# Performance work log

Measured on AMD Instinct MI355X. Metric: run time of the kernel, lower is better.

Reference implementation:

```python
import jax, jax.numpy as jnp
import numpy as np

HIDDEN = 512
X_SIZE = 128
S_SIZE = 64


def _lstm_cell(h, c, inp, Wi, Wh, bi, bh):
    # PyTorch gate order: i, f, g, o
    gates = inp @ Wi.T + bi + h @ Wh.T + bh  # [B, 4H]
    i, f, g, o = jnp.split(gates, 4, axis=-1)
    c = jax.nn.sigmoid(f) * c + jax.nn.sigmoid(i) * jnp.tanh(g)
    h = jax.nn.sigmoid(o) * jnp.tanh(c)
    return h, c


def setup_inputs() -> dict:
    key = jax.random.key(0)
    ks = jax.random.split(key, 16)
    B, T, H = 256, 512, HIDDEN
    in0 = X_SIZE + S_SIZE
    sc0 = 1.0 / np.sqrt(H)
    d = {
        "x": jax.random.normal(ks[0], (B, T, X_SIZE), jnp.float32),
        "s0": jax.random.normal(ks[1], (B, S_SIZE), jnp.float32),
        "W_ih0": jax.random.uniform(ks[2], (4 * H, in0), jnp.float32, -sc0, sc0),
        "W_hh0": jax.random.uniform(ks[3], (4 * H, H), jnp.float32, -sc0, sc0),
        "b_ih0": jax.random.uniform(ks[4], (4 * H,), jnp.float32, -sc0, sc0),
        "b_hh0": jax.random.uniform(ks[5], (4 * H,), jnp.float32, -sc0, sc0),
        "W_ih1": jax.random.uniform(ks[6], (4 * H, H), jnp.float32, -sc0, sc0),
        "W_hh1": jax.random.uniform(ks[7], (4 * H, H), jnp.float32, -sc0, sc0),
        "b_ih1": jax.random.uniform(ks[8], (4 * H,), jnp.float32, -sc0, sc0),
        "b_hh1": jax.random.uniform(ks[9], (4 * H,), jnp.float32, -sc0, sc0),
        "W_fc": jax.random.uniform(ks[10], (S_SIZE, H), jnp.float32, -sc0, sc0),
        "b_fc": jax.random.uniform(ks[11], (S_SIZE,), jnp.float32, -sc0, sc0),
        "seq_length": 512,
    }
    return d


def reference(x, s0, W_ih0, W_hh0, b_ih0, b_hh0, W_ih1, W_hh1, b_ih1, b_hh1,
              W_fc, b_fc, seq_length):
    B = x.shape[0]
    H = W_hh0.shape[1]
    zeros = jnp.zeros((B, H), x.dtype)

    def step(carry, x_t):
        h0, c0, h1, c1, s = carry
        inp = jnp.concatenate([x_t, s], axis=-1)  # [B, x_size + s_size]
        h0, c0 = _lstm_cell(h0, c0, inp, W_ih0, W_hh0, b_ih0, b_hh0)
        h1, c1 = _lstm_cell(h1, c1, h0, W_ih1, W_hh1, b_ih1, b_hh1)
        out = h1 @ W_fc.T + b_fc  # [B, s_size]
        s = s + out               # residual state update
        return (h0, c0, h1, c1, s), out

    xs = jnp.swapaxes(x[:, :seq_length], 0, 1)  # time-major [T, B, x_size]
    _, outs = jax.lax.scan(step, (zeros, zeros, zeros, zeros, s0), xs)
    return jnp.swapaxes(outs, 0, 1)  # [B, T, s_size]
```

## Files before the change

kernel.cpp:

```cpp
#include <hip/hip_runtime.h>
#include <cstdint>
#include <cstddef>

typedef __bf16 bf16;
typedef _Float16 f16;
typedef __bf16 bf16x8 __attribute__((ext_vector_type(8)));
typedef _Float16 f16x8 __attribute__((ext_vector_type(8)));
typedef float  f32x4  __attribute__((ext_vector_type(4)));
typedef unsigned int uint2v __attribute__((ext_vector_type(2)));
typedef unsigned int uint4v __attribute__((ext_vector_type(4)));
typedef unsigned long long u64;

constexpr int B_=256, T_=512, H_=512, X_=128, S_=64, IN0=192;
constexpr int NG=2;
constexpr int MG=128;
constexpr int WPG=128;
constexpr int KB_X=4, KB_H=16, KB_S=2;
constexpr float LOSCL = 4096.0f, INV_LOSCL = 1.0f/4096.0f;

constexpr size_t OFF_FLG=0;
constexpr size_t OFF_BC =16384;
constexpr size_t OFF_SC =32768;
constexpr size_t OFF_HP =OFF_SC+2ull*NG*64*128*4;
constexpr size_t PLANE  =2ull*B_*H_*2;
constexpr size_t WS_NEED=OFF_HP+2*PLANE;

constexpr int NWX=KB_X*512;
constexpr int NWH=KB_H*512;
constexpr int NWS=KB_S*512;
constexpr int SMEM_BYTES = (2*NWX + 8*NWH + 2*NWS)*2
                         + 2*512*2 + 128*17*4 + 512*2 + 32*4;
static_assert(SMEM_BYTES == 155264, "lds size");
static_assert(SMEM_BYTES <= 160*1024, "lds limit");

__device__ __forceinline__ uint4v ald16(const void* p) {
  uint4v r;
  asm volatile("global_load_dwordx4 %0, %1, off sc1"
               : "=&v"(r) : "v"(p) : "memory");
  return r;
}
__device__ __forceinline__ f16x8 MKF(uint4v q) {
  union { uint4v q; f16x8 v; } u; u.q = q;
  return u.v;
}
__device__ __forceinline__ void astore8(void* p, uint2v v) {
  union { uint2v v; u64 q; } u; u.v = v;
  __hip_atomic_store((u64*)p, u.q, __ATOMIC_RELAXED, __HIP_MEMORY_SCOPE_AGENT);
}
__device__ __forceinline__ void astoref(float* p, float v) {
  __hip_atomic_store((unsigned*)p, __float_as_uint(v), __ATOMIC_RELAXED, __HIP_MEMORY_SCOPE_AGENT);
}
__device__ __forceinline__ float aloadf(const float* p) {
  return __uint_as_float(__hip_atomic_load((unsigned*)p, __ATOMIC_RELAXED, __HIP_MEMORY_SCOPE_AGENT));
}

__device__ __forceinline__ f32x4 mfmaB(bf16x8 a, bf16x8 b, f32x4 c) {
  return __builtin_amdgcn_mfma_f32_16x16x32_bf16(a, b, c, 0, 0, 0);
}
__device__ __forceinline__ f32x4 mfmaF(f16x8 a, f16x8 b, f32x4 c) {
  return __builtin_amdgcn_mfma_f32_16x16x32_f16(a, b, c, 0, 0, 0);
}
__device__ __forceinline__ f32x4 mfma3(bf16x8 ah, bf16x8 al, bf16x8 wh, bf16x8 wl, f32x4 c) {
  c = mfmaB(ah, wh, c);
  c = mfmaB(al, wh, c);
  c = mfmaB(ah, wl, c);
  return c;
}
__device__ __forceinline__ void split8p(const float* v, bf16x8& ah, bf16x8& al) {
  #pragma unroll
  for (int i=0;i<8;++i){ float f=v[i]; bf16 h=(bf16)f; ah[i]=h; al[i]=(bf16)(f-(float)h); }
}
__device__ __forceinline__ void split8v(f32x4 v0, f32x4 v1, bf16x8& ah, bf16x8& al) {
  #pragma unroll
  for (int i=0;i<4;++i){ float f=v0[i]; bf16 h=(bf16)f; ah[i]=h; al[i]=(bf16)(f-(float)h); }
  #pragma unroll
  for (int i=0;i<4;++i){ float f=v1[i]; bf16 h=(bf16)f; ah[4+i]=h; al[4+i]=(bf16)(f-(float)h); }
}
__device__ __forceinline__ float sigm(float v) { return 1.0f / (1.0f + __expf(-v)); }
__device__ __forceinline__ float tanhr(float v) {
  v = fminf(15.0f, fmaxf(-15.0f, v));
  float e = __expf(2.0f * v);
  return (e - 1.0f) / (e + 1.0f);
}

__device__ __forceinline__ void group_barrier(int* flg, int* bc, int ns, int& phase) {
  ++phase;
  const int p = phase;
  asm volatile("s_waitcnt vmcnt(0)" ::: "memory");
  __syncthreads();
  if (threadIdx.x == 0)
    __hip_atomic_store(flg + ns*16, p, __ATOMIC_RELAXED, __HIP_MEMORY_SCOPE_AGENT);
  if (ns == 0) {
    if (threadIdx.x < WPG) {
      while (__hip_atomic_load(flg + (int)threadIdx.x*16, __ATOMIC_RELAXED,
                               __HIP_MEMORY_SCOPE_AGENT) < p)
        __builtin_amdgcn_s_sleep(1);
    }
    __syncthreads();
    if (threadIdx.x == 0)
      __hip_atomic_store(bc, p, __ATOMIC_RELAXED, __HIP_MEMORY_SCOPE_AGENT);
  }
  if (threadIdx.x == 0) {
    while (__hip_atomic_load(bc, __ATOMIC_RELAXED, __HIP_MEMORY_SCOPE_AGENT) < p)
      __builtin_amdgcn_s_sleep(1);
  }
  __syncthreads();
}

__device__ void pack_slice(bf16* dH, bf16* dL, const float* src, int stride,
                           int koff, int nkb, int ns) {
  for (int p = (int)threadIdx.x; p < nkb*64; p += 256) {
    int ln = p & 63, kb = p >> 6;
    int c = ln & 15, k = kb*32 + ((ln>>4)<<3);
    int gcol = ((c>>2)<<9) + ns*4 + (c&3);
    const float* sp = src + (size_t)gcol*stride + koff + k;
    f32x4 v0 = *(const f32x4*)sp, v1 = *(const f32x4*)(sp+4);
    bf16x8 hv, lv;
    split8v(v0, v1, hv, lv);
    *(bf16x8*)(dH + p*8) = hv;
    *(bf16x8*)(dL + p*8) = lv;
  }
}
__device__ void pack_slice_f16(f16* dH, f16* dL, const float* src, int stride,
                               int koff, int nkb, int ns) {
  for (int p = (int)threadIdx.x; p < nkb*64; p += 256) {
    int ln = p & 63, kb = p >> 6;
    int c = ln & 15, k = kb*32 + ((ln>>4)<<3);
    int gcol = ((c>>2)<<9) + ns*4 + (c&3);
    const float* sp = src + (size_t)gcol*stride + koff + k;
    f16x8 hv; f16x8 lv;
    #pragma unroll
    for (int i=0;i<8;++i) {
      float f = sp[i];
      f16 h = (f16)f;
      hv[i] = h;
      lv[i] = (f16)((f - (float)h) * LOSCL);
    }
    *(f16x8*)(dH + p*8) = hv;
    *(f16x8*)(dL + p*8) = lv;
  }
}

__global__ void zero_kernel(char* __restrict__ ws) {
  size_t i = (size_t)blockIdx.x*256 + threadIdx.x;
  size_t nsync = 32768/8;
  if (i < nsync) {
    __hip_atomic_store((u64*)(ws+OFF_FLG) + i, 0ull,
                       __ATOMIC_RELAXED, __HIP_MEMORY_SCOPE_AGENT);
    return;
  }
  i -= nsync;
  if (i < 2*PLANE/8)
    __hip_atomic_store((u64*)(ws+OFF_HP) + i, 0ull,
                       __ATOMIC_RELAXED, __HIP_MEMORY_SCOPE_AGENT);
}

#define FRB(base, kb) (*(const bf16x8*)((base) + (((kb)*64 + lane)*8)))
#define FRF(base, kb) (*(const f16x8*)((base) + (((kb)*64 + lane)*8)))
#define WFC(base, kb) (*(const f16x8*)((base) + (kb)*32 + kq))

__global__ void __launch_bounds__(256, 1)
lstm_kernel(const float* __restrict__ x, const float* __restrict__ s0,
            const float* __restrict__ Wi0, const float* __restrict__ Wh0g,
            const float* __restrict__ bi0, const float* __restrict__ bh0,
            const float* __restrict__ Wi1g, const float* __restrict__ Wh1g,
            const float* __restrict__ bi1, const float* __restrict__ bh1,
            const float* __restrict__ Wfc, const float* __restrict__ bfc,
            float* __restrict__ out, char* __restrict__ ws)
{
  const int bid = blockIdx.x;
  const int g = bid & 1, ns = bid >> 1;
  const int tid = threadIdx.x;
  const int w = tid >> 6, lane = tid & 63, l15 = lane & 15;
  const int kq = (lane >> 4) << 3;
  const int mB = g * MG;
  const bool evenNs = (ns & 1) == 0;
  const int cstar = ns >> 1;
  int rowA[2];
  rowA[0] = mB + (w*2)*16 + l15;
  rowA[1] = rowA[0] + 16;

  int* flg = (int*)(ws + OFF_FLG) + g*128*16;
  int* bc  = (int*)(ws + OFF_BC) + g*16;
  float* SCbase = (float*)(ws + OFF_SC);
  f16* H0H_ = (f16*)(ws + OFF_HP);
  f16* H1H_ = (f16*)(ws + OFF_HP + PLANE);

  extern __shared__ char smem[];
  bf16* sWxH  = (bf16*)smem;
  bf16* sWxL  = sWxH + NWX;
  f16* sWh0H = (f16*)(sWxL + NWX);
  f16* sWh0L = sWh0H + NWH;
  f16* sWcbH = sWh0L + NWH;
  f16* sWcbL = sWcbH + NWH;
  f16* sWi1H = sWcbL + NWH;
  f16* sWi1L = sWi1H + NWH;
  f16* sWh1H = sWi1L + NWH;
  f16* sWh1L = sWh1H + NWH;
  bf16* sWsH  = (bf16*)(sWh1L + NWH);
  bf16* sWsL  = sWsH + NWS;
  f16* sWfcH = (f16*)(sWsL + NWS);
  f16* sWfcL = sWfcH + 512;
  float* sG   = (float*)(sWfcL + 512);
  f16*  sHh  = (f16*)(sG + 128*17);
  float* sB0  = (float*)(sHh + 512);
  float* sB1  = sB0 + 16;

  pack_slice(sWxH,  sWxL,  Wi0,  IN0, 0,  KB_X, ns);
  pack_slice_f16(sWh0H, sWh0L, Wh0g, H_,  0,  KB_H, ns);
  pack_slice_f16(sWi1H, sWi1L, Wi1g, H_,  0,  KB_H, ns);
  pack_slice_f16(sWh1H, sWh1L, Wh1g, H_,  0,  KB_H, ns);
  pack_slice(sWsH,  sWsL,  Wi0,  IN0, X_, KB_S, ns);
  for (int p = tid; p < KB_H*64; p += 256) {
    int ln = p & 63, kb = p >> 6;
    int c = ln & 15, k = kb*32 + ((ln>>4)<<3);
    int gcol = ((c>>2)<<9) + ns*4 + (c&3);
    const float* wis = Wi0 + (size_t)gcol*IN0 + X_;
    float a[8] = {0,0,0,0,0,0,0,0};
    for (int o = 0; o < S_; ++o) {
      float wv = wis[o];
      const float* fr = Wfc + (size_t)o*H_ + k;
      f32x4 f0 = *(const f32x4*)fr, f1 = *(const f32x4*)(fr+4);
      a[0]+=wv*f0[0]; a[1]+=wv*f0[1]; a[2]+=wv*f0[2]; a[3]+=wv*f0[3];
      a[4]+=wv*f1[0]; a[5]+=wv*f1[1]; a[6]+=wv*f1[2]; a[7]+=wv*f1[3];
    }
    f16x8 hv, lv;
    #pragma unroll
    for (int i=0;i<8;++i) {
      f16 h = (f16)a[i];
      hv[i] = h;
      lv[i] = (f16)((a[i] - (float)h) * LOSCL);
    }
    *(f16x8*)(sWcbH + p*8) = hv;
    *(f16x8*)(sWcbL + p*8) = lv;
  }
  for (int j = tid; j < H_; j += 256) {
    float f = Wfc[(size_t)cstar*H_ + j];
    f16 h = (f16)f;
    sWfcH[j] = h;
    sWfcL[j] = (f16)((f - (float)h) * LOSCL);
  }
  if (tid < 16) {
    int gcol = ((tid>>2)<<9) + ns*4 + (tid&3);
    sB0[tid] = bi0[gcol] + bh0[gcol];
    sB1[tid] = bi1[gcol] + bh1[gcol];
  }

  float bfcW;
  {
    int gcol = ((l15>>2)<<9) + ns*4 + (l15&3);
    const float* wr = Wi0 + (size_t)gcol*IN0 + X_;
    float bw = 0.f;
    for (int o = 0; o < S_; ++o) bw += bfc[o]*wr[o];
    bfcW = bw;
  }
  const float bfc_ns = bfc[cstar];

  float s_reg[2][16];
  #pragma unroll
  for (int mt=0;mt<2;++mt)
    #pragma unroll
    for (int kb=0;kb<KB_S;++kb)
      #pragma unroll
      for (int i=0;i<8;++i)
        s_reg[mt][kb*8+i] = s0[(size_t)rowA[mt]*S_ + kb*32 + kq + i];

  __syncthreads();

  f32x4 Gs[2];
  #pragma unroll
  for (int mt=0;mt<2;++mt) {
    bf16x8 sh0,sl0,sh1,sl1;
    split8p(&s_reg[mt][0], sh0, sl0);
    split8p(&s_reg[mt][8], sh1, sl1);
    f32x4 a = (f32x4){0.f,0.f,0.f,0.f};
    a = mfma3(sh0, sl0, FRB(sWsH,0), FRB(sWsL,0), a);
    a = mfma3(sh1, sl1, FRB(sWsH,1), FRB(sWsL,1), a);
    Gs[mt] = a;
  }

  uint4v c0q[2][16];
  #pragma unroll
  for (int mt=0;mt<2;++mt)
    #pragma unroll
    for (int kb=0;kb<16;++kb) c0q[mt][kb] = (uint4v){0,0,0,0};

  float c0s[2] = {0.f,0.f}, c1s[2] = {0.f,0.f};
  const int crow = tid >> 1;
  const int dbase = (tid & 1) << 1;
  int phase = 0;

  for (int t = 0; t < T_; ++t) {
    const int rd = t & 1, wr = rd ^ 1;
    const size_t rdo = (size_t)rd*B_*H_, wro = (size_t)wr*B_*H_;
    float* SCp = SCbase + ((size_t)rd*NG + g)*(64*128);

    f32x4 acc0[2], acc0L[2], acc1[2], acc1L[2], accF[2], accFL[2];
    {
      float addb = (t > 0) ? bfcW : 0.f;
      #pragma unroll
      for (int mt=0;mt<2;++mt) {
        #pragma unroll
        for (int r=0;r<4;++r) acc0[mt][r] = Gs[mt][r] + addb;
        acc0L[mt] = (f32x4){0.f,0.f,0.f,0.f};
        acc1[mt]  = (f32x4){0.f,0.f,0.f,0.f};
        acc1L[mt] = (f32x4){0.f,0.f,0.f,0.f};
        accF[mt]  = (f32x4){0.f,0.f,0.f,0.f};
        accFL[mt] = (f32x4){0.f,0.f,0.f,0.f};
      }
    }
    #pragma unroll
    for (int kb=0; kb<KB_X; ++kb) {
      bf16x8 wh = FRB(sWxH,kb), wl = FRB(sWxL,kb);
      #pragma unroll
      for (int mt=0;mt<2;++mt) {
        const float* xp = x + ((size_t)rowA[mt]*T_ + t)*X_ + kb*32 + kq;
        bf16x8 ah, al2;
        split8v(*(const f32x4*)xp, *(const f32x4*)(xp+4), ah, al2);
        acc0[mt] = mfma3(ah, al2, wh, wl, acc0[mt]);
      }
    }
    #pragma unroll
    for (int hb=0; hb<2; ++hb) {
      const int kb0 = hb*8;
      uint4v q[2][8];
      #pragma unroll
      for (int mt=0;mt<2;++mt) {
        const f16* bA = H1H_ + rdo + (size_t)rowA[mt]*H_ + kb0*32 + kq;
        #pragma unroll
        for (int k=0;k<8;++k) q[mt][k] = ald16(bA + k*32);
      }
      asm volatile("s_waitcnt vmcnt(0)" ::: "memory");
      __builtin_amdgcn_sched_barrier(0);
      #pragma unroll
      for (int k=0;k<8;++k) {
        const int kb = kb0 + k;
        f16x8 cbh = FRF(sWcbH,kb), cbl = FRF(sWcbL,kb);
        f16x8 whh = FRF(sWh1H,kb), whl = FRF(sWh1L,kb);
        f16x8 fH  = WFC(sWfcH,kb),  fL = WFC(sWfcL,kb);
        #pragma unroll
        for (int mt=0;mt<2;++mt) {
          f16x8 a = MKF(q[mt][k]);
          acc0[mt]  = mfmaF(a, cbh, acc0[mt]);
          acc0L[mt] = mfmaF(a, cbl, acc0L[mt]);
          acc1[mt]  = mfmaF(a, whh, acc1[mt]);
          acc1L[mt] = mfmaF(a, whl, acc1L[mt]);
          accF[mt]  = mfmaF(a, fH,  accF[mt]);
          accFL[mt] = mfmaF(a, fL,  accFL[mt]);
        }
      }
    }
    #pragma unroll
    for (int kb=0; kb<KB_H; ++kb) {
      f16x8 wh = FRF(sWh0H,kb), wl = FRF(sWh0L,kb);
      #pragma unroll
      for (int mt=0;mt<2;++mt) {
        f16x8 a = MKF(c0q[mt][kb]);
        acc0[mt]  = mfmaF(a, wh, acc0[mt]);
        acc0L[mt] = mfmaF(a, wl, acc0L[mt]);
      }
    }
    if (t > 0 && evenNs && l15 == 0) {
      #pragma unroll
      for (int mt=0;mt<2;++mt)
        #pragma unroll
        for (int r=0;r<4;++r) {
          int rloc = (w*2+mt)*16 + ((lane>>4)<<2) + r;
          float o = accF[mt][r] + accFL[mt][r]*INV_LOSCL + bfc_ns;
          out[((size_t)(mB+rloc)*T_ + (t-1))*S_ + cstar] = o;
          astoref(&SCp[cstar*128 + rloc], o);
        }
    }

    #pragma unroll
    for (int mt=0;mt<2;++mt)
      #pragma unroll
      for (int r=0;r<4;++r)
        sG[((w*2+mt)*16 + ((lane>>4)<<2) + r)*17 + l15] =
            acc0[mt][r] + acc0L[mt][r]*INV_LOSCL;
    __syncthreads();
    {
      const float* gr = sG + crow*17;
      #pragma unroll
      for (int j=0;j<2;++j) {
        int d = dbase + j;
        float gi = gr[d]    + sB0[d];
        float gf = gr[4+d]  + sB0[4+d];
        float gg = gr[8+d]  + sB0[8+d];
        float go = gr[12+d] + sB0[12+d];
        c0s[j] = sigm(gf)*c0s[j] + sigm(gi)*tanhr(gg);
        sHh[crow*4+d] = (f16)(sigm(go)*tanhr(c0s[j]));
      }
    }
    __syncthreads();
    if (tid < MG) {
      size_t off = wro + (size_t)(mB+tid)*H_ + ns*4;
      astore8(H0H_ + off, *(const uint2v*)(sHh + tid*4));
    }
    group_barrier(flg, bc, ns, phase);

    if (t > 0) {
      const float* SCr = SCbase + ((size_t)rd*NG + g)*(64*128);
      #pragma unroll
      for (int mt=0;mt<2;++mt) {
        int rloc = (w*2+mt)*16 + l15;
        #pragma unroll
        for (int kb=0;kb<KB_S;++kb)
          #pragma unroll
          for (int i=0;i<8;++i)
            s_reg[mt][kb*8+i] += aloadf(&SCr[(kb*32+kq+i)*128 + rloc]);
      }
    }
    #pragma unroll
    for (int mt=0;mt<2;++mt) {
      bf16x8 sh0,sl0,sh1,sl1;
      split8p(&s_reg[mt][0], sh0, sl0);
      split8p(&s_reg[mt][8], sh1, sl1);
      f32x4 a = (f32x4){0.f,0.f,0.f,0.f};
      a = mfma3(sh0, sl0, FRB(sWsH,0), FRB(sWsL,0), a);
      a = mfma3(sh1, sl1, FRB(sWsH,1), FRB(sWsL,1), a);
      Gs[mt] = a;
    }

    #pragma unroll
    for (int hb=0; hb<2; ++hb) {
      const int kb0 = hb*8;
      #pragma unroll
      for (int mt=0;mt<2;++mt) {
        const f16* bA = H0H_ + wro + (size_t)rowA[mt]*H_ + kb0*32 + kq;
        #pragma unroll
        for (int k=0;k<8;++k) c0q[mt][kb0+k] = ald16(bA + k*32);
      }
      asm volatile("s_waitcnt vmcnt(0)" ::: "memory");
      __builtin_amdgcn_sched_barrier(0);
      #pragma unroll
      for (int k=0;k<8;++k) {
        const int kb = kb0 + k;
        f16x8 wh = FRF(sWi1H,kb), wl = FRF(sWi1L,kb);
        #pragma unroll
        for (int mt=0;mt<2;++mt) {
          f16x8 a = MKF(c0q[mt][kb]);
          acc1[mt]  = mfmaF(a, wh, acc1[mt]);
          acc1L[mt] = mfmaF(a, wl, acc1L[mt]);
        }
      }
    }

    #pragma unroll
    for (int mt=0;mt<2;++mt)
      #pragma unroll
      for (int r=0;r<4;++r)
        sG[((w*2+mt)*16 + ((lane>>4)<<2) + r)*17 + l15] =
            acc1[mt][r] + acc1L[mt][r]*INV_LOSCL;
    __syncthreads();
    {
      const float* gr = sG + crow*17;
      #pragma unroll
      for (int j=0;j<2;++j) {
        int d = dbase + j;
        float gi = gr[d]    + sB1[d];
        float gf = gr[4+d]  + sB1[4+d];
        float gg = gr[8+d]  + sB1[8+d];
        float go = gr[12+d] + sB1[12+d];
        c1s[j] = sigm(gf)*c1s[j] + sigm(gi)*tanhr(gg);
        sHh[crow*4+d] = (f16)(sigm(go)*tanhr(c1s[j]));
      }
    }
    __syncthreads();
    if (tid < MG) {
      size_t off = wro + (size_t)(mB+tid)*H_ + ns*4;
      astore8(H1H_ + off, *(const uint2v*)(sHh + tid*4));
    }
    group_barrier(flg, bc, ns, phase);
  }

  if (evenNs) {
    f32x4 accF[2], accFL[2];
    #pragma unroll
    for (int mt=0;mt<2;++mt) {
      accF[mt]  = (f32x4){0.f,0.f,0.f,0.f};
      accFL[mt] = (f32x4){0.f,0.f,0.f,0.f};
    }
    #pragma unroll
    for (int hb=0; hb<2; ++hb) {
      const int kb0 = hb*8;
      uint4v q[2][8];
      #pragma unroll
      for (int mt=0;mt<2;++mt) {
        const f16* bA = H1H_ + (size_t)rowA[mt]*H_ + kb0*32 + kq;
        #pragma unroll
        for (int k=0;k<8;++k) q[mt][k] = ald16(bA + k*32);
      }
      asm volatile("s_waitcnt vmcnt(0)" ::: "memory");
      __builtin_amdgcn_sched_barrier(0);
      #pragma unroll
      for (int k=0;k<8;++k) {
        const int kb = kb0 + k;
        f16x8 fH = WFC(sWfcH,kb), fL = WFC(sWfcL,kb);
        #pragma unroll
        for (int mt=0;mt<2;++mt) {
          f16x8 a = MKF(q[mt][k]);
          accF[mt]  = mfmaF(a, fH, accF[mt]);
          accFL[mt] = mfmaF(a, fL, accFL[mt]);
        }
      }
    }
    if (l15 == 0) {
      #pragma unroll
      for (int mt=0;mt<2;++mt)
        #pragma unroll
        for (int r=0;r<4;++r) {
          int rloc = (w*2+mt)*16 + ((lane>>4)<<2) + r;
          float o = accF[mt][r] + accFL[mt][r]*INV_LOSCL + bfc_ns;
          out[((size_t)(mB+rloc)*T_ + (T_-1))*S_ + cstar] = o;
        }
    }
  }
}

extern "C" void kernel_launch(void* const* d_in, const int* in_sizes, int n_in,
                              void* d_out, int out_size, void* d_ws, size_t ws_size,
                              hipStream_t stream)
{
  const float* x   = (const float*)d_in[0];
  const float* s0  = (const float*)d_in[1];
  const float* Wi0 = (const float*)d_in[2];
  const float* Wh0 = (const float*)d_in[3];
  const float* bi0 = (const float*)d_in[4];
  const float* bh0 = (const float*)d_in[5];
  const float* Wi1 = (const float*)d_in[6];
  const float* Wh1 = (const float*)d_in[7];
  const float* bi1 = (const float*)d_in[8];
  const float* bh1 = (const float*)d_in[9];
  const float* Wfc = (const float*)d_in[10];
  const float* bfc = (const float*)d_in[11];
  float* out = (float*)d_out;
  char* ws = (char*)d_ws;

  if (ws_size < WS_NEED) return;

  hipFuncSetAttribute(reinterpret_cast<const void*>(lstm_kernel),
                      hipFuncAttributeMaxDynamicSharedMemorySize, SMEM_BYTES);

  size_t nz = 32768/8 + 2*PLANE/8;
  zero_kernel<<<(int)((nz + 255)/256), 256, 0, stream>>>(ws);
  lstm_kernel<<<NG*WPG, 256, SMEM_BYTES, stream>>>(x, s0, Wi0, Wh0, bi0, bh0,
                                                   Wi1, Wh1, bi1, bh1, Wfc, bfc,
                                                   out, ws);
}
```

Before: 10.16 ms.

## Flatten group barrier and overlap hidden-state loads with MFMA work

```diff
diff --git a/kernel.cpp b/kernel.cpp
--- a/kernel.cpp
+++ b/kernel.cpp
@@ -19,7 +19,6 @@
 constexpr float LOSCL = 4096.0f, INV_LOSCL = 1.0f/4096.0f;
 
 constexpr size_t OFF_FLG=0;
-constexpr size_t OFF_BC =16384;
 constexpr size_t OFF_SC =32768;
 constexpr size_t OFF_HP =OFF_SC+2ull*NG*64*128*4;
 constexpr size_t PLANE  =2ull*B_*H_*2;
@@ -39,6 +38,8 @@
                : "=&v"(r) : "v"(p) : "memory");
   return r;
 }
+#define VMW0 do { asm volatile("s_waitcnt vmcnt(0)" ::: "memory"); \
+                  __builtin_amdgcn_sched_barrier(0); } while (0)
 __device__ __forceinline__ f16x8 MKF(uint4v q) {
   union { uint4v q; f16x8 v; } u; u.q = q;
   return u.v;
@@ -83,25 +84,16 @@
   return (e - 1.0f) / (e + 1.0f);
 }
 
-__device__ __forceinline__ void group_barrier(int* flg, int* bc, int ns, int& phase) {
+__device__ __forceinline__ void group_barrier(int* flg, int ns, int& phase) {
   ++phase;
   const int p = phase;
   asm volatile("s_waitcnt vmcnt(0)" ::: "memory");
   __syncthreads();
   if (threadIdx.x == 0)
     __hip_atomic_store(flg + ns*16, p, __ATOMIC_RELAXED, __HIP_MEMORY_SCOPE_AGENT);
-  if (ns == 0) {
-    if (threadIdx.x < WPG) {
-      while (__hip_atomic_load(flg + (int)threadIdx.x*16, __ATOMIC_RELAXED,
-                               __HIP_MEMORY_SCOPE_AGENT) < p)
-        __builtin_amdgcn_s_sleep(1);
-    }
-    __syncthreads();
-    if (threadIdx.x == 0)
-      __hip_atomic_store(bc, p, __ATOMIC_RELAXED, __HIP_MEMORY_SCOPE_AGENT);
-  }
-  if (threadIdx.x == 0) {
-    while (__hip_atomic_load(bc, __ATOMIC_RELAXED, __HIP_MEMORY_SCOPE_AGENT) < p)
+  if (threadIdx.x < WPG) {
+    while (__hip_atomic_load(flg + (int)threadIdx.x*16, __ATOMIC_RELAXED,
+                             __HIP_MEMORY_SCOPE_AGENT) < p)
       __builtin_amdgcn_s_sleep(1);
   }
   __syncthreads();
@@ -181,7 +173,6 @@
   rowA[1] = rowA[0] + 16;
 
   int* flg = (int*)(ws + OFF_FLG) + g*128*16;
-  int* bc  = (int*)(ws + OFF_BC) + g*16;
   float* SCbase = (float*)(ws + OFF_SC);
   f16* H0H_ = (f16*)(ws + OFF_HP);
   f16* H1H_ = (f16*)(ws + OFF_HP + PLANE);
@@ -320,35 +311,12 @@
         acc0[mt] = mfma3(ah, al2, wh, wl, acc0[mt]);
       }
     }
-    #pragma unroll
-    for (int hb=0; hb<2; ++hb) {
-      const int kb0 = hb*8;
-      uint4v q[2][8];
-      #pragma unroll
-      for (int mt=0;mt<2;++mt) {
-        const f16* bA = H1H_ + rdo + (size_t)rowA[mt]*H_ + kb0*32 + kq;
-        #pragma unroll
-        for (int k=0;k<8;++k) q[mt][k] = ald16(bA + k*32);
-      }
-      asm volatile("s_waitcnt vmcnt(0)" ::: "memory");
-      __builtin_amdgcn_sched_barrier(0);
-      #pragma unroll
-      for (int k=0;k<8;++k) {
-        const int kb = kb0 + k;
-        f16x8 cbh = FRF(sWcbH,kb), cbl = FRF(sWcbL,kb);
-        f16x8 whh = FRF(sWh1H,kb), whl = FRF(sWh1L,kb);
-        f16x8 fH  = WFC(sWfcH,kb),  fL = WFC(sWfcL,kb);
-        #pragma unroll
-        for (int mt=0;mt<2;++mt) {
-          f16x8 a = MKF(q[mt][k]);
-          acc0[mt]  = mfmaF(a, cbh, acc0[mt]);
-          acc0L[mt] = mfmaF(a, cbl, acc0L[mt]);
-          acc1[mt]  = mfmaF(a, whh, acc1[mt]);
-          acc1L[mt] = mfmaF(a, whl, acc1L[mt]);
-          accF[mt]  = mfmaF(a, fH,  accF[mt]);
-          accFL[mt] = mfmaF(a, fL,  accFL[mt]);
-        }
-      }
+    uint4v q1a[2][8], q1b[2][8];
+    #pragma unroll
+    for (int mt=0;mt<2;++mt) {
+      const f16* bA = H1H_ + rdo + (size_t)rowA[mt]*H_ + kq;
+      #pragma unroll
+      for (int k=0;k<8;++k) q1a[mt][k] = ald16(bA + k*32);
     }
     #pragma unroll
     for (int kb=0; kb<KB_H; ++kb) {
@@ -358,6 +326,48 @@
         f16x8 a = MKF(c0q[mt][kb]);
         acc0[mt]  = mfmaF(a, wh, acc0[mt]);
         acc0L[mt] = mfmaF(a, wl, acc0L[mt]);
+      }
+    }
+    VMW0;
+    #pragma unroll
+    for (int mt=0;mt<2;++mt) {
+      const f16* bA = H1H_ + rdo + (size_t)rowA[mt]*H_ + kq + 256;
+      #pragma unroll
+      for (int k=0;k<8;++k) q1b[mt][k] = ald16(bA + k*32);
+    }
+    #pragma unroll
+    for (int k=0;k<8;++k) {
+      const int kb = k;
+      f16x8 cbh = FRF(sWcbH,kb), cbl = FRF(sWcbL,kb);
+      f16x8 whh = FRF(sWh1H,kb), whl = FRF(sWh1L,kb);
+      f16x8 fH  = WFC(sWfcH,kb),  fL = WFC(sWfcL,kb);
+      #pragma unroll
+      for (int mt=0;mt<2;++mt) {
+        f16x8 a = MKF(q1a[mt][k]);
+        acc0[mt]  = mfmaF(a, cbh, acc0[mt]);
+        acc0L[mt] = mfmaF(a, cbl, acc0L[mt]);
+        acc1[mt]  = mfmaF(a, whh, acc1[mt]);
+        acc1L[mt] = mfmaF(a, whl, acc1L[mt]);
+        accF[mt]  = mfmaF(a, fH,  accF[mt]);
+        accFL[mt] = mfmaF(a, fL,  accFL[mt]);
+      }
+    }
+    VMW0;
+    #pragma unroll
+    for (int k=0;k<8;++k) {
+      const int kb = 8 + k;
+      f16x8 cbh = FRF(sWcbH,kb), cbl = FRF(sWcbL,kb);
+      f16x8 whh = FRF(sWh1H,kb), whl = FRF(sWh1L,kb);
+      f16x8 fH  = WFC(sWfcH,kb),  fL = WFC(sWfcL,kb);
+      #pragma unroll
+      for (int mt=0;mt<2;++mt) {
+        f16x8 a = MKF(q1b[mt][k]);
+        acc0[mt]  = mfmaF(a, cbh, acc0[mt]);
+        acc0L[mt] = mfmaF(a, cbl, acc0L[mt]);
+        acc1[mt]  = mfmaF(a, whh, acc1[mt]);
+        acc1L[mt] = mfmaF(a, whl, acc1L[mt]);
+        accF[mt]  = mfmaF(a, fH,  accF[mt]);
+        accFL[mt] = mfmaF(a, fL,  accFL[mt]);
       }
     }
     if (t > 0 && evenNs && l15 == 0) {
@@ -397,7 +407,7 @@
       size_t off = wro + (size_t)(mB+tid)*H_ + ns*4;
       astore8(H0H_ + off, *(const uint2v*)(sHh + tid*4));
     }
-    group_barrier(flg, bc, ns, phase);
+    group_barrier(flg, ns, phase);
 
     if (t > 0) {
       const float* SCr = SCbase + ((size_t)rd*NG + g)*(64*128);
@@ -410,6 +420,12 @@
           for (int i=0;i<8;++i)
             s_reg[mt][kb*8+i] += aloadf(&SCr[(kb*32+kq+i)*128 + rloc]);
       }
+    }
+    #pragma unroll
+    for (int mt=0;mt<2;++mt) {
+      const f16* bA = H0H_ + wro + (size_t)rowA[mt]*H_ + kq;
+      #pragma unroll
+      for (int k=0;k<8;++k) c0q[mt][k] = ald16(bA + k*32);
     }
     #pragma unroll
     for (int mt=0;mt<2;++mt) {
@@ -421,28 +437,32 @@
       a = mfma3(sh1, sl1, FRB(sWsH,1), FRB(sWsL,1), a);
       Gs[mt] = a;
     }
-
-    #pragma unroll
-    for (int hb=0; hb<2; ++hb) {
-      const int kb0 = hb*8;
-      #pragma unroll
-      for (int mt=0;mt<2;++mt) {
-        const f16* bA = H0H_ + wro + (size_t)rowA[mt]*H_ + kb0*32 + kq;
-        #pragma unroll
-        for (int k=0;k<8;++k) c0q[mt][kb0+k] = ald16(bA + k*32);
-      }
-      asm volatile("s_waitcnt vmcnt(0)" ::: "memory");
-      __builtin_amdgcn_sched_barrier(0);
-      #pragma unroll
-      for (int k=0;k<8;++k) {
-        const int kb = kb0 + k;
-        f16x8 wh = FRF(sWi1H,kb), wl = FRF(sWi1L,kb);
-        #pragma unroll
-        for (int mt=0;mt<2;++mt) {
-          f16x8 a = MKF(c0q[mt][kb]);
-          acc1[mt]  = mfmaF(a, wh, acc1[mt]);
-          acc1L[mt] = mfmaF(a, wl, acc1L[mt]);
-        }
+    VMW0;
+    #pragma unroll
+    for (int mt=0;mt<2;++mt) {
+      const f16* bA = H0H_ + wro + (size_t)rowA[mt]*H_ + kq + 256;
+      #pragma unroll
+      for (int k=0;k<8;++k) c0q[mt][8+k] = ald16(bA + k*32);
+    }
+    #pragma unroll
+    for (int kb=0; kb<8; ++kb) {
+      f16x8 wh = FRF(sWi1H,kb), wl = FRF(sWi1L,kb);
+      #pragma unroll
+      for (int mt=0;mt<2;++mt) {
+        f16x8 a = MKF(c0q[mt][kb]);
+        acc1[mt]  = mfmaF(a, wh, acc1[mt]);
+        acc1L[mt] = mfmaF(a, wl, acc1L[mt]);
+      }
+    }
+    VMW0;
+    #pragma unroll
+    for (int kb=8; kb<16; ++kb) {
+      f16x8 wh = FRF(sWi1H,kb), wl = FRF(sWi1L,kb);
+      #pragma unroll
+      for (int mt=0;mt<2;++mt) {
+        f16x8 a = MKF(c0q[mt][kb]);
+        acc1[mt]  = mfmaF(a, wh, acc1[mt]);
+        acc1L[mt] = mfmaF(a, wl, acc1L[mt]);
       }
     }
 
@@ -471,7 +491,7 @@
       size_t off = wro + (size_t)(mB+tid)*H_ + ns*4;
       astore8(H1H_ + off, *(const uint2v*)(sHh + tid*4));
     }
-    group_barrier(flg, bc, ns, phase);
+    group_barrier(flg, ns, phase);
   }
 
   if (evenNs) {
@@ -481,28 +501,22 @@
       accF[mt]  = (f32x4){0.f,0.f,0.f,0.f};
       accFL[mt] = (f32x4){0.f,0.f,0.f,0.f};
     }
-    #pragma unroll
-    for (int hb=0; hb<2; ++hb) {
-      const int kb0 = hb*8;
-      uint4v q[2][8];
-      #pragma unroll
-      for (int mt=0;mt<2;++mt) {
-        const f16* bA = H1H_ + (size_t)rowA[mt]*H_ + kb0*32 + kq;
-        #pragma unroll
-        for (int k=0;k<8;++k) q[mt][k] = ald16(bA + k*32);
-      }
-      asm volatile("s_waitcnt vmcnt(0)" ::: "memory");
-      __builtin_amdgcn_sched_barrier(0);
-      #pragma unroll
-      for (int k=0;k<8;++k) {
-        const int kb = kb0 + k;
-        f16x8 fH = WFC(sWfcH,kb), fL = WFC(sWfcL,kb);
-        #pragma unroll
-        for (int mt=0;mt<2;++mt) {
-          f16x8 a = MKF(q[mt][k]);
-          accF[mt]  = mfmaF(a, fH, accF[mt]);
-          accFL[mt] = mfmaF(a, fL, accFL[mt]);
-        }
+    uint4v q[2][16];
+    #pragma unroll
+    for (int mt=0;mt<2;++mt) {
+      const f16* bA = H1H_ + (size_t)rowA[mt]*H_ + kq;
+      #pragma unroll
+      for (int kb=0; kb<16; ++kb) q[mt][kb] = ald16(bA + kb*32);
+    }
+    VMW0;
+    #pragma unroll
+    for (int kb=0; kb<16; ++kb) {
+      f16x8 fH = WFC(sWfcH,kb), fL = WFC(sWfcL,kb);
+      #pragma unroll
+      for (int mt=0;mt<2;++mt) {
+        f16x8 a = MKF(q[mt][kb]);
+        accF[mt]  = mfmaF(a, fH, accF[mt]);
+        accFL[mt] = mfmaF(a, fL, accFL[mt]);
       }
     }
     if (l15 == 0) {
```

After: 9.425 ms. 1.08x faster.
